# Optimization experiments

Measured on AMD Instinct MI355X. Metric: run time of the kernel, lower is better.

## Reference

```python
import jax, jax.numpy as jnp
import numpy as np

B, E, T, H = 4, 16, 1024, 1024
NEG = -10000.0


def setup_inputs() -> dict:
    key = jax.random.key(0)
    ks = jax.random.split(key, 9)
    s = 1.0 / np.sqrt(H)
    return {
        "token_embedding": jax.random.normal(ks[0], (B, T, H), jnp.float32),
        "entity_embedding": jax.random.normal(ks[1], (B, E, H), jnp.float32),
        "token_mask": jax.random.bernoulli(ks[2], 0.9, (B, T)),
        "Wt": jax.random.normal(ks[3], (H, H), jnp.float32) * s,
        "bt": jax.random.normal(ks[4], (H,), jnp.float32) * s,
        "We": jax.random.normal(ks[5], (H, H), jnp.float32) * s,
        "be": jax.random.normal(ks[6], (H,), jnp.float32) * s,
        "Wp": jax.random.normal(ks[7], (H,), jnp.float32) * s,
        "bp": jax.random.normal(ks[8], (1,), jnp.float32) * s,
    }


def reference(token_embedding, entity_embedding, token_mask, Wt, bt, We, be, Wp, bp):
    # token branch: [B,T,H] @ [H,H] -> [B,T,H]
    t = jnp.einsum('bth,hk->btk', token_embedding, Wt) + bt
    # entity branch: [B,E,H] @ [H,H] -> [B,E,H]
    e = jnp.einsum('beh,hk->bek', entity_embedding, We) + be
    # broadcast add -> relu -> linear-to-scalar: [B,E,T,H] -> [B,E,T]
    m = jax.nn.relu(t[:, None, :, :] + e[:, :, None, :])
    cls = jnp.einsum('beth,h->bet', m, Wp) + bp[0]
    # mask fill (after squeeze, per squeeze=True path)
    cls = jnp.where(token_mask[:, None, :], cls, NEG)
    p = jax.nn.sigmoid(cls)
    return cls, p
```

## Files before the change

kernel.cpp:

```cpp
#include <hip/hip_runtime.h>

typedef unsigned short us;
typedef __attribute__((ext_vector_type(8))) short short8;
typedef __attribute__((ext_vector_type(4))) float f32x4;

__device__ __forceinline__ us f2bf(float f) {
  unsigned int u = __builtin_bit_cast(unsigned int, f);
  u += 0x7fffu + ((u >> 16) & 1u);
  return (us)(u >> 16);
}

__device__ __forceinline__ void gload_lds16(const void* g, void* l) {
  __builtin_amdgcn_global_load_lds(
      (const __attribute__((address_space(1))) void*)g,
      (__attribute__((address_space(3))) void*)l, 16, 0, 0);
}

__global__ __launch_bounds__(256) void prep_kernel(
    const float* __restrict__ token, us* __restrict__ tokb,
    const float* __restrict__ Wt, us* __restrict__ WtT,
    const float* __restrict__ entity, const float* __restrict__ We,
    float* __restrict__ epart) {
  __shared__ float tile[64][65];
  __shared__ float eS[16][128];
  const int bid = blockIdx.x, tid = threadIdx.x;
  if (bid < 4096) {
    int q = bid * 256 + tid;
    float4 v = ((const float4*)token)[q];
    ushort4 o;
    o.x = f2bf(v.x); o.y = f2bf(v.y); o.z = f2bf(v.z); o.w = f2bf(v.w);
    ((ushort4*)tokb)[q] = o;
  } else if (bid < 4352) {
    int tb = bid - 4096;
    int bx = (tb & 15) << 6, by = ((tb >> 4) & 15) << 6;
    int r0 = tid >> 4, c0 = (tid & 15) << 2;
#pragma unroll
    for (int p = 0; p < 4; ++p) {
      int r = p * 16 + r0;
      float4 v = *(const float4*)&Wt[(size_t)(by + r) * 1024 + bx + c0];
      tile[r][c0] = v.x; tile[r][c0 + 1] = v.y;
      tile[r][c0 + 2] = v.z; tile[r][c0 + 3] = v.w;
    }
    __syncthreads();
#pragma unroll
    for (int p = 0; p < 4; ++p) {
      int r = p * 16 + r0;
      ushort4 o;
      o.x = f2bf(tile[c0 + 0][r]); o.y = f2bf(tile[c0 + 1][r]);
      o.z = f2bf(tile[c0 + 2][r]); o.w = f2bf(tile[c0 + 3][r]);
      *(ushort4*)&WtT[(size_t)(bx + r) * 1024 + by + c0] = o;
    }
  } else {
    int eb = bid - 4352;
    int kc = eb & 7, nt = (eb >> 3) & 7, b = eb >> 6;
    int k0 = kc << 7, n0 = nt << 7;
#pragma unroll
    for (int p = 0; p < 2; ++p) {
      int idx = (p << 8) + tid;
      int r = idx >> 5, kk = (idx & 31) << 2;
      *(float4*)&eS[r][kk] = *(const float4*)&entity[(size_t)(((b << 4) + r) << 10) + k0 + kk];
    }
    __syncthreads();
    const int col = tid & 127, rh = tid >> 7;
    const float* wP = We + ((size_t)k0 << 10) + n0 + col;
    float acc[8] = {0.f, 0.f, 0.f, 0.f, 0.f, 0.f, 0.f, 0.f};
#pragma unroll 8
    for (int k = 0; k < 128; ++k) {
      float wv = wP[(size_t)k << 10];
#pragma unroll
      for (int r = 0; r < 8; ++r)
        acc[r] = fmaf(wv, eS[(rh << 3) + r][k], acc[r]);
    }
    float* op = epart + (((size_t)((kc << 6) + (b << 4) + (rh << 3))) << 10) + n0 + col;
#pragma unroll
    for (int r = 0; r < 8; ++r) op[(size_t)r << 10] = acc[r];
  }
}

__global__ __launch_bounds__(256) void main_kernel(
    const us* __restrict__ tokb, const us* __restrict__ WtT,
    const float* __restrict__ epart, const float* __restrict__ be,
    const float* __restrict__ bt, const float* __restrict__ wp,
    float* __restrict__ partial) {
  __shared__ __attribute__((aligned(16))) us Ws[4096];
  __shared__ __attribute__((aligned(16))) us Ts[4096];
  __shared__ __attribute__((aligned(16))) float eL[16][132];
  __shared__ __attribute__((aligned(16))) float btL[128];
  __shared__ __attribute__((aligned(16))) float wpL[128];
  __shared__ float pp[2][128][17];
  const int tid = threadIdx.x;
  const int mh = blockIdx.x, tt = blockIdx.y;
  const int h0 = mh << 7, b = tt >> 3;
#pragma unroll
  for (int p = 0; p < 2; ++p) {
    int q = (p << 8) + tid;
    int er = q >> 5, ec = (q & 31) << 2;
    f32x4 s = *(const f32x4*)&be[h0 + ec];
#pragma unroll
    for (int kc = 0; kc < 8; ++kc)
      s += *(const f32x4*)&epart[(((size_t)((kc << 6) + (b << 4) + er)) << 10) + h0 + ec];
    *(f32x4*)&eL[er][ec] = s;
  }
  if (tid < 128) btL[tid] = bt[h0 + tid];
  else wpL[tid - 128] = wp[h0 + tid - 128];
  const int row1 = tid >> 2, kc4 = (tid & 3) << 3;
  const us* wP = WtT + (size_t)(h0 + row1) * 1024 + kc4;
  const us* tP = tokb + (size_t)((tt << 7) + row1) * 1024 + kc4;
  const int w = tid >> 6;
  us* wL = &Ws[w * 512];
  us* tL = &Ts[w * 512];
  const int lane = tid & 63, wm = (tid >> 7) & 1, wn = (tid >> 6) & 1;
  const int l16 = lane & 15, oct = lane >> 4, ko = oct << 3;
  int wfo[4], tfo[4];
#pragma unroll
  for (int i = 0; i < 4; ++i) {
    wfo[i] = (((wm << 6) + (i << 4) + l16) << 5) + ko;
    tfo[i] = (((wn << 6) + (i << 4) + l16) << 5) + ko;
  }
  f32x4 acc[4][4] = {};
  for (int kt = 0; kt < 32; ++kt) {
    const int ko2 = kt << 5;
    __syncthreads();
    gload_lds16(wP + ko2, wL); gload_lds16(wP + 65536 + ko2, wL + 2048);
    gload_lds16(tP + ko2, tL); gload_lds16(tP + 65536 + ko2, tL + 2048);
    __syncthreads();
    short8 af[4], bfr[4];
#pragma unroll
    for (int i = 0; i < 4; ++i) af[i] = *(const short8*)&Ws[wfo[i]];
#pragma unroll
    for (int j = 0; j < 4; ++j) bfr[j] = *(const short8*)&Ts[tfo[j]];
#pragma unroll
    for (int i = 0; i < 4; ++i)
#pragma unroll
      for (int j = 0; j < 4; ++j)
        acc[i][j] = __builtin_amdgcn_mfma_f32_16x16x32_bf16(af[i], bfr[j], acc[i][j], 0, 0, 0);
  }
  f32x4 btq[4], wpq[4];
#pragma unroll
  for (int i = 0; i < 4; ++i) {
    int hb = (wm << 6) + (i << 4) + (oct << 2);
    btq[i] = *(const f32x4*)&btL[hb];
    wpq[i] = *(const f32x4*)&wpL[hb];
  }
#pragma unroll
  for (int i = 0; i < 4; ++i)
#pragma unroll
    for (int j = 0; j < 4; ++j) acc[i][j] += btq[i];
#pragma unroll
  for (int e = 0; e < 16; ++e) {
    f32x4 ev[4];
#pragma unroll
    for (int i = 0; i < 4; ++i)
      ev[i] = *(const f32x4*)&eL[e][(wm << 6) + (i << 4) + (oct << 2)];
    float pj[4] = {0.f, 0.f, 0.f, 0.f};
#pragma unroll
    for (int j = 0; j < 4; ++j)
#pragma unroll
      for (int i = 0; i < 4; ++i)
#pragma unroll
        for (int r = 0; r < 4; ++r)
          pj[j] = fmaf(fmaxf(acc[i][j][r] + ev[i][r], 0.f), wpq[i][r], pj[j]);
#pragma unroll
    for (int j = 0; j < 4; ++j) {
      pj[j] += __shfl_xor(pj[j], 16, 64);
      pj[j] += __shfl_xor(pj[j], 32, 64);
    }
    if (oct == 0) {
#pragma unroll
      for (int j = 0; j < 4; ++j) pp[wm][(wn << 6) + (j << 4) + l16][e] = pj[j];
    }
  }
  __syncthreads();
#pragma unroll
  for (int q = 0; q < 8; ++q) {
    int flat = (q << 8) + tid;
    int e = flat >> 7, tl = flat & 127;
    float v = pp[0][tl][e] + pp[1][tl][e];
    partial[((size_t)mh << 16) + (size_t)((((b << 4) + e) << 10) + ((tt & 7) << 7) + tl)] = v;
  }
}

__global__ __launch_bounds__(256) void finalize_kernel(
    const float* __restrict__ partial, const float* __restrict__ bp,
    const int* __restrict__ mask, float* __restrict__ out) {
  int idx = blockIdx.x * 256 + threadIdx.x;
  float s = 0.f;
#pragma unroll
  for (int mh = 0; mh < 8; ++mh) s += partial[((size_t)mh << 16) + idx];
  float cls = s + bp[0];
  int b = idx >> 14, t = idx & 1023;
  if (mask[(b << 10) + t] == 0) cls = -10000.0f;
  float p = 1.0f / (1.0f + __expf(-cls));
  out[idx] = cls;
  out[65536 + idx] = p;
}

extern "C" void kernel_launch(void* const* d_in, const int* in_sizes, int n_in,
                              void* d_out, int out_size, void* d_ws, size_t ws_size,
                              hipStream_t stream) {
  const float* token = (const float*)d_in[0];
  const float* entity = (const float*)d_in[1];
  const int* mask = (const int*)d_in[2];
  const float* Wt = (const float*)d_in[3];
  const float* bt = (const float*)d_in[4];
  const float* We = (const float*)d_in[5];
  const float* be = (const float*)d_in[6];
  const float* Wp = (const float*)d_in[7];
  const float* bp = (const float*)d_in[8];
  float* out = (float*)d_out;

  char* ws = (char*)d_ws;
  us* tokb = (us*)ws;
  us* WtT = tokb + (size_t)4096 * 1024;
  float* epart = (float*)(WtT + (size_t)1024 * 1024);
  float* partial = epart + (size_t)8 * 64 * 1024;

  prep_kernel<<<4608, 256, 0, stream>>>(token, tokb, Wt, WtT, entity, We, epart);
  main_kernel<<<dim3(8, 32), 256, 0, stream>>>(tokb, WtT, epart, be, bt, Wp, partial);
  finalize_kernel<<<256, 256, 0, stream>>>(partial, bp, mask, out);
}
```

Measured before the change: 124.1 us.

## Double-buffer LDS tiles in main GEMM, halve token tile, reorder prep blocks

The main kernel now prefetches the next K-slices into a second LDS buffer using async global-to-LDS loads with explicit waitcnt and barriers, so loads overlap with MFMA work. The token tile per block shrinks from 128 to 64 rows, doubling the grid to 512 blocks for better CU occupancy. The prep kernel moves the slow entity-GEMM blocks to the front so they are scheduled first. The cost is a smaller per-block tile with less reuse, plus the risk of subtle synchronisation errors from the hand-written waitcnt.

```diff
diff --git a/kernel.cpp b/kernel.cpp
--- a/kernel.cpp
+++ b/kernel.cpp
@@ -24,35 +24,8 @@
   __shared__ float tile[64][65];
   __shared__ float eS[16][128];
   const int bid = blockIdx.x, tid = threadIdx.x;
-  if (bid < 4096) {
-    int q = bid * 256 + tid;
-    float4 v = ((const float4*)token)[q];
-    ushort4 o;
-    o.x = f2bf(v.x); o.y = f2bf(v.y); o.z = f2bf(v.z); o.w = f2bf(v.w);
-    ((ushort4*)tokb)[q] = o;
-  } else if (bid < 4352) {
-    int tb = bid - 4096;
-    int bx = (tb & 15) << 6, by = ((tb >> 4) & 15) << 6;
-    int r0 = tid >> 4, c0 = (tid & 15) << 2;
-#pragma unroll
-    for (int p = 0; p < 4; ++p) {
-      int r = p * 16 + r0;
-      float4 v = *(const float4*)&Wt[(size_t)(by + r) * 1024 + bx + c0];
-      tile[r][c0] = v.x; tile[r][c0 + 1] = v.y;
-      tile[r][c0 + 2] = v.z; tile[r][c0 + 3] = v.w;
-    }
-    __syncthreads();
-#pragma unroll
-    for (int p = 0; p < 4; ++p) {
-      int r = p * 16 + r0;
-      ushort4 o;
-      o.x = f2bf(tile[c0 + 0][r]); o.y = f2bf(tile[c0 + 1][r]);
-      o.z = f2bf(tile[c0 + 2][r]); o.w = f2bf(tile[c0 + 3][r]);
-      *(ushort4*)&WtT[(size_t)(bx + r) * 1024 + by + c0] = o;
-    }
-  } else {
-    int eb = bid - 4352;
-    int kc = eb & 7, nt = (eb >> 3) & 7, b = eb >> 6;
+  if (bid < 256) {
+    int kc = bid & 7, nt = (bid >> 3) & 7, b = bid >> 6;
     int k0 = kc << 7, n0 = nt << 7;
 #pragma unroll
     for (int p = 0; p < 2; ++p) {
@@ -74,6 +47,32 @@
     float* op = epart + (((size_t)((kc << 6) + (b << 4) + (rh << 3))) << 10) + n0 + col;
 #pragma unroll
     for (int r = 0; r < 8; ++r) op[(size_t)r << 10] = acc[r];
+  } else if (bid < 4352) {
+    int q = (bid - 256) * 256 + tid;
+    float4 v = ((const float4*)token)[q];
+    ushort4 o;
+    o.x = f2bf(v.x); o.y = f2bf(v.y); o.z = f2bf(v.z); o.w = f2bf(v.w);
+    ((ushort4*)tokb)[q] = o;
+  } else {
+    int tb = bid - 4352;
+    int bx = (tb & 15) << 6, by = ((tb >> 4) & 15) << 6;
+    int r0 = tid >> 4, c0 = (tid & 15) << 2;
+#pragma unroll
+    for (int p = 0; p < 4; ++p) {
+      int r = p * 16 + r0;
+      float4 v = *(const float4*)&Wt[(size_t)(by + r) * 1024 + bx + c0];
+      tile[r][c0] = v.x; tile[r][c0 + 1] = v.y;
+      tile[r][c0 + 2] = v.z; tile[r][c0 + 3] = v.w;
+    }
+    __syncthreads();
+#pragma unroll
+    for (int p = 0; p < 4; ++p) {
+      int r = p * 16 + r0;
+      ushort4 o;
+      o.x = f2bf(tile[c0 + 0][r]); o.y = f2bf(tile[c0 + 1][r]);
+      o.z = f2bf(tile[c0 + 2][r]); o.w = f2bf(tile[c0 + 3][r]);
+      *(ushort4*)&WtT[(size_t)(bx + r) * 1024 + by + c0] = o;
+    }
   }
 }
 
@@ -82,15 +81,15 @@
     const float* __restrict__ epart, const float* __restrict__ be,
     const float* __restrict__ bt, const float* __restrict__ wp,
     float* __restrict__ partial) {
-  __shared__ __attribute__((aligned(16))) us Ws[4096];
-  __shared__ __attribute__((aligned(16))) us Ts[4096];
+  __shared__ __attribute__((aligned(16))) us Ws[2][4096];
+  __shared__ __attribute__((aligned(16))) us Ts[2][2048];
   __shared__ __attribute__((aligned(16))) float eL[16][132];
   __shared__ __attribute__((aligned(16))) float btL[128];
   __shared__ __attribute__((aligned(16))) float wpL[128];
-  __shared__ float pp[2][128][17];
+  __shared__ float pp[2][64][17];
   const int tid = threadIdx.x;
   const int mh = blockIdx.x, tt = blockIdx.y;
-  const int h0 = mh << 7, b = tt >> 3;
+  const int h0 = mh << 7, b = tt >> 4, t0 = (tt & 15) << 6;
 #pragma unroll
   for (int p = 0; p < 2; ++p) {
     int q = (p << 8) + tid;
@@ -103,37 +102,49 @@
   }
   if (tid < 128) btL[tid] = bt[h0 + tid];
   else wpL[tid - 128] = wp[h0 + tid - 128];
+  asm volatile("" ::: "memory");
   const int row1 = tid >> 2, kc4 = (tid & 3) << 3;
   const us* wP = WtT + (size_t)(h0 + row1) * 1024 + kc4;
-  const us* tP = tokb + (size_t)((tt << 7) + row1) * 1024 + kc4;
+  const us* tP = tokb + (size_t)((b << 10) + t0 + row1) * 1024 + kc4;
   const int w = tid >> 6;
-  us* wL = &Ws[w * 512];
-  us* tL = &Ts[w * 512];
+  us* w0 = &Ws[0][w * 512]; us* w1 = &Ws[1][w * 512];
+  us* t0L = &Ts[0][w * 512]; us* t1L = &Ts[1][w * 512];
+  gload_lds16(wP, w0); gload_lds16(wP + 65536, w0 + 2048);
+  gload_lds16(tP, t0L);
+  gload_lds16(wP + 32, w1); gload_lds16(wP + 65536 + 32, w1 + 2048);
+  gload_lds16(tP + 32, t1L);
   const int lane = tid & 63, wm = (tid >> 7) & 1, wn = (tid >> 6) & 1;
   const int l16 = lane & 15, oct = lane >> 4, ko = oct << 3;
-  int wfo[4], tfo[4];
-#pragma unroll
-  for (int i = 0; i < 4; ++i) {
-    wfo[i] = (((wm << 6) + (i << 4) + l16) << 5) + ko;
-    tfo[i] = (((wn << 6) + (i << 4) + l16) << 5) + ko;
-  }
-  f32x4 acc[4][4] = {};
+  int wfo[4], tfo[2];
+#pragma unroll
+  for (int i = 0; i < 4; ++i) wfo[i] = (((wm << 6) + (i << 4) + l16) << 5) + ko;
+#pragma unroll
+  for (int j = 0; j < 2; ++j) tfo[j] = (((wn << 5) + (j << 4) + l16) << 5) + ko;
+  f32x4 acc[4][2] = {};
   for (int kt = 0; kt < 32; ++kt) {
-    const int ko2 = kt << 5;
-    __syncthreads();
-    gload_lds16(wP + ko2, wL); gload_lds16(wP + 65536 + ko2, wL + 2048);
-    gload_lds16(tP + ko2, tL); gload_lds16(tP + 65536 + ko2, tL + 2048);
-    __syncthreads();
-    short8 af[4], bfr[4];
-#pragma unroll
-    for (int i = 0; i < 4; ++i) af[i] = *(const short8*)&Ws[wfo[i]];
-#pragma unroll
-    for (int j = 0; j < 4; ++j) bfr[j] = *(const short8*)&Ts[tfo[j]];
+    const us* Wb = Ws[kt & 1];
+    const us* Tb = Ts[kt & 1];
+    __builtin_amdgcn_s_waitcnt(0x0f73);
+    __builtin_amdgcn_s_barrier();
+    asm volatile("" ::: "memory");
+    short8 af[4], bfr[2];
+#pragma unroll
+    for (int i = 0; i < 4; ++i) af[i] = *(const short8*)&Wb[wfo[i]];
+#pragma unroll
+    for (int j = 0; j < 2; ++j) bfr[j] = *(const short8*)&Tb[tfo[j]];
 #pragma unroll
     for (int i = 0; i < 4; ++i)
 #pragma unroll
-      for (int j = 0; j < 4; ++j)
+      for (int j = 0; j < 2; ++j)
         acc[i][j] = __builtin_amdgcn_mfma_f32_16x16x32_bf16(af[i], bfr[j], acc[i][j], 0, 0, 0);
+    asm volatile("" ::: "memory");
+    __builtin_amdgcn_s_barrier();
+    int nk = kt + 2; if (nk > 31) nk = 30;
+    int ko2 = nk << 5;
+    us* dw = (kt & 1) ? w1 : w0;
+    us* dt = (kt & 1) ? t1L : t0L;
+    gload_lds16(wP + ko2, dw); gload_lds16(wP + 65536 + ko2, dw + 2048);
+    gload_lds16(tP + ko2, dt);
   }
   f32x4 btq[4], wpq[4];
 #pragma unroll
@@ -145,38 +156,38 @@
 #pragma unroll
   for (int i = 0; i < 4; ++i)
 #pragma unroll
-    for (int j = 0; j < 4; ++j) acc[i][j] += btq[i];
+    for (int j = 0; j < 2; ++j) acc[i][j] += btq[i];
 #pragma unroll
   for (int e = 0; e < 16; ++e) {
     f32x4 ev[4];
 #pragma unroll
     for (int i = 0; i < 4; ++i)
       ev[i] = *(const f32x4*)&eL[e][(wm << 6) + (i << 4) + (oct << 2)];
-    float pj[4] = {0.f, 0.f, 0.f, 0.f};
-#pragma unroll
-    for (int j = 0; j < 4; ++j)
+    float pj[2] = {0.f, 0.f};
+#pragma unroll
+    for (int j = 0; j < 2; ++j)
 #pragma unroll
       for (int i = 0; i < 4; ++i)
 #pragma unroll
         for (int r = 0; r < 4; ++r)
           pj[j] = fmaf(fmaxf(acc[i][j][r] + ev[i][r], 0.f), wpq[i][r], pj[j]);
 #pragma unroll
-    for (int j = 0; j < 4; ++j) {
+    for (int j = 0; j < 2; ++j) {
       pj[j] += __shfl_xor(pj[j], 16, 64);
       pj[j] += __shfl_xor(pj[j], 32, 64);
     }
     if (oct == 0) {
 #pragma unroll
-      for (int j = 0; j < 4; ++j) pp[wm][(wn << 6) + (j << 4) + l16][e] = pj[j];
+      for (int j = 0; j < 2; ++j) pp[wm][(wn << 5) + (j << 4) + l16][e] = pj[j];
     }
   }
   __syncthreads();
 #pragma unroll
-  for (int q = 0; q < 8; ++q) {
+  for (int q = 0; q < 4; ++q) {
     int flat = (q << 8) + tid;
-    int e = flat >> 7, tl = flat & 127;
+    int e = flat >> 6, tl = flat & 63;
     float v = pp[0][tl][e] + pp[1][tl][e];
-    partial[((size_t)mh << 16) + (size_t)((((b << 4) + e) << 10) + ((tt & 7) << 7) + tl)] = v;
+    partial[((size_t)mh << 16) + (size_t)((((b << 4) + e) << 10) + t0 + tl)] = v;
   }
 }
 
@@ -216,6 +227,6 @@
   float* partial = epart + (size_t)8 * 64 * 1024;
 
   prep_kernel<<<4608, 256, 0, stream>>>(token, tokb, Wt, WtT, entity, We, epart);
-  main_kernel<<<dim3(8, 32), 256, 0, stream>>>(tokb, WtT, epart, be, bt, Wp, partial);
+  main_kernel<<<dim3(8, 64), 256, 0, stream>>>(tokb, WtT, epart, be, bt, Wp, partial);
   finalize_kernel<<<256, 256, 0, stream>>>(partial, bp, mask, out);
 }
```

New measurement: 114.0 us. -8.1%, faster.
